# Kernel optimization log

Measured on AMD Instinct MI355X. Metric: run time of the kernel, lower is better.

Reference implementation:

```python
import jax, jax.numpy as jnp
import numpy as np

N_NODES = 32
N_EDGES = N_NODES * (N_NODES - 1)  # 992
BATCH = 16
SEQ = 8
BS = BATCH * SEQ  # 128 frames
D = 256  # node_latent_dim == edge_latent_dim
ITERS = 3


def gru_cell(x, h, Wih, Whh, bih, bhh):
    # torch GRUCell: gates ordered (r, z, n)
    gi = x @ Wih.T + bih
    gh = h @ Whh.T + bhh
    ir, iz, inn = jnp.split(gi, 3, axis=-1)
    hr, hz, hn = jnp.split(gh, 3, axis=-1)
    r = jax.nn.sigmoid(ir + hr)
    z = jax.nn.sigmoid(iz + hz)
    n = jnp.tanh(inn + r * hn)
    return (1.0 - z) * n + z * h


def setup_inputs() -> dict:
    key = jax.random.key(0)
    ks = jax.random.split(key, 16)
    s = 0.05
    inp = {
        'node_latents': jax.random.normal(ks[0], (BS * N_NODES, D), jnp.float32),
        'edge_latents': jax.random.normal(ks[1], (BS * N_EDGES, D), jnp.float32),
        'node_Wih': jax.random.normal(ks[2], (3 * D, D), jnp.float32) * s,
        'node_Whh': jax.random.normal(ks[3], (3 * D, D), jnp.float32) * s,
        'node_bih': jax.random.normal(ks[4], (3 * D,), jnp.float32) * s,
        'node_bhh': jax.random.normal(ks[5], (3 * D,), jnp.float32) * s,
        'edge_Wih': jax.random.normal(ks[6], (3 * D, D), jnp.float32) * s,
        'edge_Whh': jax.random.normal(ks[7], (3 * D, D), jnp.float32) * s,
        'edge_bih': jax.random.normal(ks[8], (3 * D,), jnp.float32) * s,
        'edge_bhh': jax.random.normal(ks[9], (3 * D,), jnp.float32) * s,
        'w_node_pool': jax.random.normal(ks[10], (2 * D,), jnp.float32) * s,
        'w_edge_pool_sub': jax.random.normal(ks[11], (2 * D,), jnp.float32) * s,
        'w_edge_pool_obj': jax.random.normal(ks[12], (2 * D,), jnp.float32) * s,
    }
    # all ordered (subject, object) pairs with subject != object, same for every frame
    pairs = np.array([(i, j) for i in range(N_NODES) for j in range(N_NODES) if i != j], dtype=np.int32)  # [E,2]
    e2n = np.concatenate([np.arange(N_EDGES, dtype=np.int32)[:, None], pairs], axis=1)  # [E,3]
    inp['edge_idx_to_node_idxs'] = jnp.asarray(np.broadcast_to(e2n, (BS, N_EDGES, 3)).copy())
    return inp


def reference(node_latents, edge_latents, node_Wih, node_Whh, node_bih, node_bhh,
              edge_Wih, edge_Whh, edge_bih, edge_bhh,
              w_node_pool, w_edge_pool_sub, w_edge_pool_obj, edge_idx_to_node_idxs):
    sub = edge_idx_to_node_idxs[..., 1].astype(jnp.int32)  # [BS,E]
    obj = edge_idx_to_node_idxs[..., 2].astype(jnp.int32)
    bidx = jnp.arange(BS, dtype=jnp.int32)[:, None]
    sub_flat = (bidx * N_NODES + sub).reshape(-1)  # [BS*E]
    obj_flat = (bidx * N_NODES + obj).reshape(-1)

    # initial GRU call with zero hidden state (torch GRUCell default)
    node_hidden = gru_cell(node_latents, jnp.zeros_like(node_latents), node_Wih, node_Whh, node_bih, node_bhh)
    edge_hidden = gru_cell(edge_latents, jnp.zeros_like(edge_latents), edge_Wih, edge_Whh, edge_bih, edge_bhh)

    for _ in range(ITERS):
        nh = node_hidden.reshape(BS, N_NODES, D)
        eh = edge_hidden.reshape(BS, N_EDGES, D)
        ns = jnp.take_along_axis(nh, sub[:, :, None], axis=1)  # [BS,E,D] subject node feats
        no = jnp.take_along_axis(nh, obj[:, :, None], axis=1)  # [BS,E,D]
        cat_s = jnp.concatenate([ns, eh], axis=-1)  # [BS,E,2D]
        cat_o = jnp.concatenate([no, eh], axis=-1)
        g_node = jax.nn.sigmoid(cat_s @ w_node_pool)[..., None]        # [BS,E,1]
        g_sub = jax.nn.sigmoid(cat_s @ w_edge_pool_sub)[..., None]
        g_obj = jax.nn.sigmoid(cat_o @ w_edge_pool_obj)[..., None]
        # node message: gated edge features scattered to subject and object nodes
        # (equivalent to the dense 0/1 incidence matmul since subject != object per edge)
        msg_e = (g_node * eh).reshape(-1, D)  # [BS*E,D]
        node_msg = (jax.ops.segment_sum(msg_e, sub_flat, num_segments=BS * N_NODES)
                    + jax.ops.segment_sum(msg_e, obj_flat, num_segments=BS * N_NODES))  # [BS*N,D]
        edge_msg = (g_sub * ns + g_obj * no).reshape(-1, D)  # [BS*E,D]
        node_hidden = gru_cell(node_msg, node_hidden, node_Wih, node_Whh, node_bih, node_bhh)
        edge_hidden = gru_cell(edge_msg, edge_hidden, edge_Wih, edge_Whh, edge_bih, edge_bhh)

    return (node_hidden.reshape(BS, N_NODES, D), edge_hidden.reshape(BS, N_EDGES, D))
```

## Files before the change

### kernel.cpp

```cpp
#include <hip/hip_runtime.h>


#define D_DIM 256
#define NNODE 32
#define NEDGE 992
#define EDGE_ROWS (128 * NEDGE)
#define NODE_ROWS (128 * NNODE)
#define BM 64
#define XH_OFF 0
#define HH_OFF 512
#define GI_OFF 32768
#define GI_STR 776

typedef _Float16 half8 __attribute__((ext_vector_type(8)));
typedef __attribute__((ext_vector_type(4))) float f32x4;

__device__ __forceinline__ float sigf(float x) { return 1.0f / (1.0f + __expf(-x)); }
__device__ __forceinline__ float tanh_fast(float x) { return 2.0f / (1.0f + __expf(-2.0f * x)) - 1.0f; }
__device__ __forceinline__ float dot4(float4 a, float4 b) { return a.x*b.x + a.y*b.y + a.z*b.z + a.w*b.w; }

__global__ __launch_bounds__(64) void pack_w(const float* __restrict__ Wih,
                                             const float* __restrict__ Whh,
                                             _Float16* __restrict__ ph) {
  const int ct = blockIdx.x;
  const int ks = blockIdx.y;
  const int l = threadIdx.x;
  const int col = ct * 16 + (l & 15);
  const int kb = ks * 32 + (l >> 4) * 8;
  const float* src = (kb < 256) ? (Wih + col * 256 + kb) : (Whh + col * 256 + (kb - 256));
  half8 v;
  #pragma unroll
  for (int j = 0; j < 8; ++j) v[j] = (_Float16)src[j];
  *(half8*)(ph + ((ct * 16 + ks) * 64 + l) * 8) = v;
}

template <int MODE>
__global__ __launch_bounds__(1024, 4) void gru_mfma(
    const float* __restrict__ xsrc, float* __restrict__ h,
    const _Float16* __restrict__ wp,
    const float* __restrict__ bih, const float* __restrict__ bhh,
    const float* __restrict__ wesb, const float* __restrict__ weob,
    const float* __restrict__ dotS, const float* __restrict__ dotO,
    _Float16* __restrict__ nw) {
  constexpr int RSTR = (MODE == 1) ? 1024 : 512;
  constexpr int LDSB = (MODE == 1) ? 65536 : (MODE == 2 ? 32768 + BM * GI_STR * 2 : 32768);
  __shared__ __align__(16) unsigned char lds[LDSB];

  const int t = threadIdx.x;
  const int rb = blockIdx.x * BM;
  const int srow = t >> 4;
  const int skc = t & 15;
  const int w = t >> 6;
  const int l = t & 63;
  const int lq = l >> 4;
  const int lr = l & 15;
  const int swm = (lr & 7) << 4;
  const int swz = (srow & 7) << 4;
  const int rowg = rb + srow;

  if constexpr (MODE == 2) {
    const int b = rowg / NEDGE;
    const int e = rowg - b * NEDGE;
    const int si = e / 31;
    const int m = e - si * 31;
    const int ob = (m < si) ? m : (m + 1);

    float4 pre[4];
    #pragma unroll
    for (int i = 0; i < 4; ++i)
      pre[i] = *(const float4*)(h + rowg * D_DIM + (i >> 1) * 128 + skc * 8 + (i & 1) * 4);
    #pragma unroll
    for (int c = 0; c < 2; ++c) {
      half8 hh8;
      const float* f1 = (const float*)&pre[c * 2];
      #pragma unroll
      for (int j = 0; j < 8; ++j) hh8[j] = (_Float16)f1[j];
      *(half8*)(&lds[(srow * 512 + c * 256 + skc * 16) ^ swz]) = hh8;
    }
    float pS = 0.f, pO = 0.f;
    #pragma unroll
    for (int i = 0; i < 4; ++i) {
      const int k0 = (i >> 1) * 128 + skc * 8 + (i & 1) * 4;
      pS += dot4(pre[i], *(const float4*)(wesb + k0));
      pO += dot4(pre[i], *(const float4*)(weob + k0));
    }
    #pragma unroll
    for (int mm = 1; mm < 16; mm <<= 1) {
      pS += __shfl_xor(pS, mm, 16);
      pO += __shfl_xor(pO, mm, 16);
    }
    const float gs = sigf(dotS[b * NNODE + si] + pS);
    const float go = sigf(dotO[b * NNODE + ob] + pO);
    const _Float16 gsh = (_Float16)gs, goh = (_Float16)go;
    const _Float16* ns = nw + (b * NNODE + si) * 768;
    const _Float16* no_ = nw + (b * NNODE + ob) * 768;
    _Float16* giw = (_Float16*)(lds + GI_OFF) + srow * GI_STR;
    #pragma unroll
    for (int j = 0; j < 6; ++j) {
      const int c0 = skc * 8 + j * 128;
      const half8 a = *(const half8*)(ns + c0);
      const half8 bb = *(const half8*)(no_ + c0);
      half8 g;
      #pragma unroll
      for (int k = 0; k < 8; ++k) g[k] = gsh * a[k] + goh * bb[k];
      *(half8*)(giw + c0) = g;
    }
  } else if constexpr (MODE != 1) {
    #pragma unroll
    for (int c = 0; c < 2; ++c) {
      half8 hx;
      #pragma unroll
      for (int pq = 0; pq < 2; ++pq) {
        const float4 a = *(const float4*)(xsrc + rowg * D_DIM + c * 128 + skc * 8 + pq * 4);
        hx[pq * 4 + 0] = (_Float16)a.x; hx[pq * 4 + 1] = (_Float16)a.y;
        hx[pq * 4 + 2] = (_Float16)a.z; hx[pq * 4 + 3] = (_Float16)a.w;
      }
      *(half8*)(&lds[(srow * 512 + c * 256 + skc * 16) ^ swz]) = hx;
    }
  } else {
    float4 pre[4];
    #pragma unroll
    for (int i = 0; i < 4; ++i)
      pre[i] = *(const float4*)(h + rowg * D_DIM + (i >> 1) * 128 + skc * 8 + (i & 1) * 4);
    #pragma unroll
    for (int c = 0; c < 2; ++c) {
      half8 hh8;
      const float* f1 = (const float*)&pre[c * 2];
      #pragma unroll
      for (int j = 0; j < 8; ++j) hh8[j] = (_Float16)f1[j];
      *(half8*)(&lds[(srow * RSTR + HH_OFF + c * 256 + skc * 16) ^ swz]) = hh8;
    }
  }

  const f32x4 zz = {0.f, 0.f, 0.f, 0.f};
  f32x4 acc_r[4] = {zz, zz, zz, zz};
  f32x4 acc_z[4] = {zz, zz, zz, zz};
  f32x4 acc_nx[4] = {zz, zz, zz, zz};
  f32x4 acc_nh[4] = {zz, zz, zz, zz};

  auto KS = [&](int hoff, int ksgl, int ksg, f32x4 (&accn)[4]) {
    half8 ah[4];
    #pragma unroll
    for (int rf = 0; rf < 4; ++rf)
      ah[rf] = *(const half8*)(&lds[((rf * 16 + lr) * RSTR + hoff + ksgl * 64 + lq * 16) ^ swm]);
    const half8 br_ = *(const half8*)(wp + (((0 * 16 + w) * 16 + ksg) * 64 + l) * 8);
    const half8 bz_ = *(const half8*)(wp + (((1 * 16 + w) * 16 + ksg) * 64 + l) * 8);
    const half8 bn_ = *(const half8*)(wp + (((2 * 16 + w) * 16 + ksg) * 64 + l) * 8);
    #pragma unroll
    for (int rf = 0; rf < 4; ++rf)
      acc_r[rf] = __builtin_amdgcn_mfma_f32_16x16x32_f16(ah[rf], br_, acc_r[rf], 0, 0, 0);
    #pragma unroll
    for (int rf = 0; rf < 4; ++rf)
      acc_z[rf] = __builtin_amdgcn_mfma_f32_16x16x32_f16(ah[rf], bz_, acc_z[rf], 0, 0, 0);
    #pragma unroll
    for (int rf = 0; rf < 4; ++rf)
      accn[rf] = __builtin_amdgcn_mfma_f32_16x16x32_f16(ah[rf], bn_, accn[rf], 0, 0, 0);
  };

  __syncthreads();

  if constexpr (MODE == 0 || MODE == 3) {
    #pragma unroll
    for (int ksgl = 0; ksgl < 8; ++ksgl) KS(0, ksgl, ksgl, acc_nx);
  } else if constexpr (MODE == 2) {
    #pragma unroll
    for (int ksgl = 0; ksgl < 8; ++ksgl) KS(0, ksgl, 8 + ksgl, acc_nh);
  } else {
    #pragma unroll
    for (int ksgl = 0; ksgl < 8; ++ksgl) KS(HH_OFF, ksgl, 8 + ksgl, acc_nh);
    #pragma unroll
    for (int c = 0; c < 2; ++c) {
      half8 hx;
      #pragma unroll
      for (int pq = 0; pq < 2; ++pq) {
        const float4 a = *(const float4*)(xsrc + rowg * D_DIM + c * 128 + skc * 8 + pq * 4);
        hx[pq * 4 + 0] = (_Float16)a.x; hx[pq * 4 + 1] = (_Float16)a.y;
        hx[pq * 4 + 2] = (_Float16)a.z; hx[pq * 4 + 3] = (_Float16)a.w;
      }
      *(half8*)(&lds[(srow * RSTR + XH_OFF + c * 256 + skc * 16) ^ swz]) = hx;
    }
    __syncthreads();
    #pragma unroll
    for (int ksgl = 0; ksgl < 8; ++ksgl) KS(XH_OFF, ksgl, ksgl, acc_nx);
  }

  const int col = w * 16 + lr;
  if constexpr (MODE == 3) {
    #pragma unroll
    for (int rf = 0; rf < 4; ++rf) {
      #pragma unroll
      for (int q = 0; q < 4; ++q) {
        const int rowl = rf * 16 + lq * 4 + q;
        _Float16* np = nw + (rb + rowl) * 768 + col;
        np[0]   = (_Float16)acc_r[rf][q];
        np[256] = (_Float16)acc_z[rf][q];
        np[512] = (_Float16)acc_nx[rf][q];
      }
    }
    return;
  }
  const float br = bih[col] + bhh[col];
  const float bz = bih[256 + col] + bhh[256 + col];
  const float bnx = bih[512 + col];
  const float bnh = bhh[512 + col];
  if constexpr (MODE == 2) {
    const _Float16* gir = (const _Float16*)(lds + GI_OFF);
    #pragma unroll
    for (int rf = 0; rf < 4; ++rf) {
      #pragma unroll
      for (int q = 0; q < 4; ++q) {
        const int rowl = rf * 16 + lq * 4 + q;
        const _Float16* gp = gir + rowl * GI_STR + col;
        const float r = sigf(acc_r[rf][q] + (float)gp[0] + br);
        const float z = sigf(acc_z[rf][q] + (float)gp[256] + bz);
        const float n = tanh_fast((float)gp[512] + bnx + r * (acc_nh[rf][q] + bnh));
        const float hv = h[(rb + rowl) * D_DIM + col];
        h[(rb + rowl) * D_DIM + col] = (1.0f - z) * n + z * hv;
      }
    }
  } else {
    #pragma unroll
    for (int rf = 0; rf < 4; ++rf) {
      #pragma unroll
      for (int q = 0; q < 4; ++q) {
        const int rowl = rf * 16 + lq * 4 + q;
        const float r = sigf(acc_r[rf][q] + br);
        const float z = sigf(acc_z[rf][q] + bz);
        const float n = tanh_fast(acc_nx[rf][q] + bnx + r * (acc_nh[rf][q] + bnh));
        float hv = 0.0f;
        if constexpr (MODE == 1) hv = h[(rb + rowl) * D_DIM + col];
        h[(rb + rowl) * D_DIM + col] = (1.0f - z) * n + z * hv;
      }
    }
  }
}

__global__ __launch_bounds__(256) void dot3_kernel(
    const float* __restrict__ nh, const float* __restrict__ wnp,
    const float* __restrict__ wes, const float* __restrict__ weo,
    float* __restrict__ dA, float* __restrict__ dS, float* __restrict__ dO) {
  const int r = blockIdx.x * 4 + (threadIdx.x >> 6);
  const int l = threadIdx.x & 63;
  const float4 v = ((const float4*)(nh + r * D_DIM))[l];
  float p1 = dot4(v, ((const float4*)wnp)[l]);
  float p2 = dot4(v, ((const float4*)wes)[l]);
  float p3 = dot4(v, ((const float4*)weo)[l]);
  #pragma unroll
  for (int mm = 32; mm > 0; mm >>= 1) {
    p1 += __shfl_xor(p1, mm, 64);
    p2 += __shfl_xor(p2, mm, 64);
    p3 += __shfl_xor(p3, mm, 64);
  }
  if (l == 0) { dA[r] = p1; dS[r] = p2; dO[r] = p3; }
}

__global__ __launch_bounds__(256) void node_msg_kernel(
    const float* __restrict__ eh, const float* __restrict__ wnp,
    const float* __restrict__ dotA, float* __restrict__ nmsg) {
  __shared__ float sh[3][256];
  const int nr = blockIdx.x;
  const int b = nr >> 5;
  const int n = nr & 31;
  const int wv = threadIdx.x >> 6;
  const int l = threadIdx.x & 63;
  const int base = b * NEDGE;
  const float4 w1b = ((const float4*)(wnp + 256))[l];

  float4 acc = {0.f, 0.f, 0.f, 0.f};
  for (int k = wv; k < 62; k += 4) {
    int e, sub;
    if (k < 31) {
      e = base + n * 31 + k;
      sub = n;
    } else {
      int i = k - 31;
      const int ip = (i < n) ? i : (i + 1);
      e = base + ip * 31 + ((n < ip) ? n : (n - 1));
      sub = ip;
    }
    const float4 ev = ((const float4*)(eh + e * D_DIM))[l];
    float p = dot4(ev, w1b);
    #pragma unroll
    for (int mm = 32; mm > 0; mm >>= 1) p += __shfl_xor(p, mm, 64);
    const float gN = sigf(dotA[b * NNODE + sub] + p);
    acc.x += gN * ev.x; acc.y += gN * ev.y; acc.z += gN * ev.z; acc.w += gN * ev.w;
  }
  if (wv > 0) *(float4*)(&sh[wv - 1][l * 4]) = acc;
  __syncthreads();
  if (wv == 0) {
    #pragma unroll
    for (int v = 0; v < 3; ++v) {
      const float4 o = *(const float4*)(&sh[v][l * 4]);
      acc.x += o.x; acc.y += o.y; acc.z += o.z; acc.w += o.w;
    }
    *(float4*)(nmsg + nr * D_DIM + l * 4) = acc;
  }
}

extern "C" void kernel_launch(void* const* d_in, const int* in_sizes, int n_in,
                              void* d_out, int out_size, void* d_ws, size_t ws_size,
                              hipStream_t stream) {
  const float* node_latents = (const float*)d_in[0];
  const float* edge_latents = (const float*)d_in[1];
  const float* node_Wih = (const float*)d_in[2];
  const float* node_Whh = (const float*)d_in[3];
  const float* node_bih = (const float*)d_in[4];
  const float* node_bhh = (const float*)d_in[5];
  const float* edge_Wih = (const float*)d_in[6];
  const float* edge_Whh = (const float*)d_in[7];
  const float* edge_bih = (const float*)d_in[8];
  const float* edge_bhh = (const float*)d_in[9];
  const float* w_node_pool = (const float*)d_in[10];
  const float* w_edge_sub = (const float*)d_in[11];
  const float* w_edge_obj = (const float*)d_in[12];

  float* nh = (float*)d_out;
  float* eh = (float*)d_out + NODE_ROWS * D_DIM;

  const int WPLANE = 48 * 16 * 64 * 8;
  _Float16* ph_n = (_Float16*)d_ws;
  _Float16* ph_e = ph_n + WPLANE;
  _Float16* NW = ph_e + WPLANE;
  float* fw = (float*)(NW + NODE_ROWS * 768);
  float* dotA = fw; fw += NODE_ROWS;
  float* dotS = fw; fw += NODE_ROWS;
  float* dotO = fw; fw += NODE_ROWS;
  float* node_msg = fw; fw += NODE_ROWS * D_DIM;

  dim3 pg(48, 16);
  pack_w<<<pg, 64, 0, stream>>>(node_Wih, node_Whh, ph_n);
  pack_w<<<pg, 64, 0, stream>>>(edge_Wih, edge_Whh, ph_e);

  gru_mfma<0><<<NODE_ROWS / BM, 1024, 0, stream>>>(
      node_latents, nh, ph_n, node_bih, node_bhh,
      nullptr, nullptr, nullptr, nullptr, nullptr);
  gru_mfma<0><<<EDGE_ROWS / BM, 1024, 0, stream>>>(
      edge_latents, eh, ph_e, edge_bih, edge_bhh,
      nullptr, nullptr, nullptr, nullptr, nullptr);

  for (int it = 0; it < 3; ++it) {
    dot3_kernel<<<NODE_ROWS / 4, 256, 0, stream>>>(nh, w_node_pool, w_edge_sub,
                                                   w_edge_obj, dotA, dotS, dotO);
    gru_mfma<3><<<NODE_ROWS / BM, 1024, 0, stream>>>(
        nh, nullptr, ph_e, nullptr, nullptr,
        nullptr, nullptr, nullptr, nullptr, NW);
    node_msg_kernel<<<NODE_ROWS, 256, 0, stream>>>(eh, w_node_pool, dotA, node_msg);
    gru_mfma<2><<<EDGE_ROWS / BM, 1024, 0, stream>>>(
        nullptr, eh, ph_e, edge_bih, edge_bhh,
        w_edge_sub + 256, w_edge_obj + 256, dotS, dotO, NW);
    gru_mfma<1><<<NODE_ROWS / BM, 1024, 0, stream>>>(
        node_msg, nh, ph_n, node_bih, node_bhh,
        nullptr, nullptr, nullptr, nullptr, nullptr);
  }
}
```

Before: 744.0 us.

## Merge node/edge GRU launches into combined grids and fuse pooling dots

The edge and node initial GRU launches become one grid, and the per-iteration edge and node GRU updates become one grid with a block-index branch. The pooling dot products move into the node-weight projection kernel, so the separate dot3 kernel goes away. This removes several launches per iteration and lets the small node work run alongside the large edge work. In exchange, the combined kernel reserves the larger edge LDS footprint for node blocks too, which may lower occupancy, and the branches add code size.

Result: faster. 715.6 us (-3.8%).

```diff
diff --git a/kernel.cpp b/kernel.cpp
--- a/kernel.cpp
+++ b/kernel.cpp
@@ -7,8 +7,8 @@
 #define EDGE_ROWS (128 * NEDGE)
 #define NODE_ROWS (128 * NNODE)
 #define BM 64
-#define XH_OFF 0
-#define HH_OFF 512
+#define EGRID (EDGE_ROWS / BM)
+#define NGRID (NODE_ROWS / BM)
 #define GI_OFF 32768
 #define GI_STR 776
 
@@ -34,18 +34,96 @@
   *(half8*)(ph + ((ct * 16 + ks) * 64 + l) * 8) = v;
 }
 
-template <int MODE>
-__global__ __launch_bounds__(1024, 4) void gru_mfma(
-    const float* __restrict__ xsrc, float* __restrict__ h,
-    const _Float16* __restrict__ wp,
-    const float* __restrict__ bih, const float* __restrict__ bhh,
-    const float* __restrict__ wesb, const float* __restrict__ weob,
-    const float* __restrict__ dotS, const float* __restrict__ dotO,
-    _Float16* __restrict__ nw) {
-  constexpr int RSTR = (MODE == 1) ? 1024 : 512;
-  constexpr int LDSB = (MODE == 1) ? 65536 : (MODE == 2 ? 32768 + BM * GI_STR * 2 : 32768);
-  __shared__ __align__(16) unsigned char lds[LDSB];
-
+__global__ __launch_bounds__(1024, 4) void gru_init(
+    const float* __restrict__ xe, const float* __restrict__ xn,
+    float* __restrict__ he, float* __restrict__ hn,
+    const _Float16* __restrict__ wpe, const _Float16* __restrict__ wpn,
+    const float* __restrict__ ebih, const float* __restrict__ ebhh,
+    const float* __restrict__ nbih, const float* __restrict__ nbhh) {
+  __shared__ __align__(16) unsigned char lds[32768];
+  const bool edge = blockIdx.x < EGRID;
+  const int bx = edge ? blockIdx.x : (blockIdx.x - EGRID);
+  const float* xsrc = edge ? xe : xn;
+  float* h = edge ? he : hn;
+  const _Float16* wp = edge ? wpe : wpn;
+  const float* bih = edge ? ebih : nbih;
+  const float* bhh = edge ? ebhh : nbhh;
+
+  const int t = threadIdx.x;
+  const int rb = bx * BM;
+  const int srow = t >> 4;
+  const int skc = t & 15;
+  const int w = t >> 6;
+  const int l = t & 63;
+  const int lq = l >> 4;
+  const int lr = l & 15;
+  const int swm = (lr & 7) << 4;
+  const int swz = (srow & 7) << 4;
+  const int rowg = rb + srow;
+
+  #pragma unroll
+  for (int c = 0; c < 2; ++c) {
+    half8 hx;
+    #pragma unroll
+    for (int pq = 0; pq < 2; ++pq) {
+      const float4 a = *(const float4*)(xsrc + rowg * D_DIM + c * 128 + skc * 8 + pq * 4);
+      hx[pq * 4 + 0] = (_Float16)a.x; hx[pq * 4 + 1] = (_Float16)a.y;
+      hx[pq * 4 + 2] = (_Float16)a.z; hx[pq * 4 + 3] = (_Float16)a.w;
+    }
+    *(half8*)(&lds[(srow * 512 + c * 256 + skc * 16) ^ swz]) = hx;
+  }
+  __syncthreads();
+
+  const f32x4 zz = {0.f, 0.f, 0.f, 0.f};
+  f32x4 acc_r[4] = {zz, zz, zz, zz};
+  f32x4 acc_z[4] = {zz, zz, zz, zz};
+  f32x4 acc_nx[4] = {zz, zz, zz, zz};
+
+  #pragma unroll
+  for (int ksg = 0; ksg < 8; ++ksg) {
+    half8 ah[4];
+    #pragma unroll
+    for (int rf = 0; rf < 4; ++rf)
+      ah[rf] = *(const half8*)(&lds[((rf * 16 + lr) * 512 + ksg * 64 + lq * 16) ^ swm]);
+    const half8 br_ = *(const half8*)(wp + (((0 * 16 + w) * 16 + ksg) * 64 + l) * 8);
+    const half8 bz_ = *(const half8*)(wp + (((1 * 16 + w) * 16 + ksg) * 64 + l) * 8);
+    const half8 bn_ = *(const half8*)(wp + (((2 * 16 + w) * 16 + ksg) * 64 + l) * 8);
+    #pragma unroll
+    for (int rf = 0; rf < 4; ++rf)
+      acc_r[rf] = __builtin_amdgcn_mfma_f32_16x16x32_f16(ah[rf], br_, acc_r[rf], 0, 0, 0);
+    #pragma unroll
+    for (int rf = 0; rf < 4; ++rf)
+      acc_z[rf] = __builtin_amdgcn_mfma_f32_16x16x32_f16(ah[rf], bz_, acc_z[rf], 0, 0, 0);
+    #pragma unroll
+    for (int rf = 0; rf < 4; ++rf)
+      acc_nx[rf] = __builtin_amdgcn_mfma_f32_16x16x32_f16(ah[rf], bn_, acc_nx[rf], 0, 0, 0);
+  }
+
+  const int col = w * 16 + lr;
+  const float br = bih[col] + bhh[col];
+  const float bz = bih[256 + col] + bhh[256 + col];
+  const float bnx = bih[512 + col];
+  const float bnh = bhh[512 + col];
+  #pragma unroll
+  for (int rf = 0; rf < 4; ++rf) {
+    #pragma unroll
+    for (int q = 0; q < 4; ++q) {
+      const int rowl = rf * 16 + lq * 4 + q;
+      const float r = sigf(acc_r[rf][q] + br);
+      const float z = sigf(acc_z[rf][q] + bz);
+      const float n = tanh_fast(acc_nx[rf][q] + bnx + r * bnh);
+      h[(rb + rowl) * D_DIM + col] = (1.0f - z) * n;
+    }
+  }
+}
+
+__global__ __launch_bounds__(1024, 4) void gru_nw(
+    const float* __restrict__ nh, const _Float16* __restrict__ wp,
+    _Float16* __restrict__ nw,
+    const float* __restrict__ wnp, const float* __restrict__ wes,
+    const float* __restrict__ weo,
+    float* __restrict__ dA, float* __restrict__ dS, float* __restrict__ dO) {
+  __shared__ __align__(16) unsigned char lds[32768];
   const int t = threadIdx.x;
   const int rb = blockIdx.x * BM;
   const int srow = t >> 4;
@@ -58,7 +136,104 @@
   const int swz = (srow & 7) << 4;
   const int rowg = rb + srow;
 
-  if constexpr (MODE == 2) {
+  float4 xa[4];
+  #pragma unroll
+  for (int i = 0; i < 4; ++i)
+    xa[i] = *(const float4*)(nh + rowg * D_DIM + (i >> 1) * 128 + skc * 8 + (i & 1) * 4);
+  #pragma unroll
+  for (int c = 0; c < 2; ++c) {
+    half8 hx;
+    const float* f0 = (const float*)&xa[c * 2];
+    #pragma unroll
+    for (int j = 0; j < 8; ++j) hx[j] = (_Float16)f0[j];
+    *(half8*)(&lds[(srow * 512 + c * 256 + skc * 16) ^ swz]) = hx;
+  }
+  float p1 = 0.f, p2 = 0.f, p3 = 0.f;
+  #pragma unroll
+  for (int i = 0; i < 4; ++i) {
+    const int k0 = (i >> 1) * 128 + skc * 8 + (i & 1) * 4;
+    p1 += dot4(xa[i], *(const float4*)(wnp + k0));
+    p2 += dot4(xa[i], *(const float4*)(wes + k0));
+    p3 += dot4(xa[i], *(const float4*)(weo + k0));
+  }
+  #pragma unroll
+  for (int mm = 1; mm < 16; mm <<= 1) {
+    p1 += __shfl_xor(p1, mm, 16);
+    p2 += __shfl_xor(p2, mm, 16);
+    p3 += __shfl_xor(p3, mm, 16);
+  }
+  if (skc == 0) { dA[rowg] = p1; dS[rowg] = p2; dO[rowg] = p3; }
+  __syncthreads();
+
+  const f32x4 zz = {0.f, 0.f, 0.f, 0.f};
+  f32x4 acc_r[4] = {zz, zz, zz, zz};
+  f32x4 acc_z[4] = {zz, zz, zz, zz};
+  f32x4 acc_nx[4] = {zz, zz, zz, zz};
+
+  #pragma unroll
+  for (int ksg = 0; ksg < 8; ++ksg) {
+    half8 ah[4];
+    #pragma unroll
+    for (int rf = 0; rf < 4; ++rf)
+      ah[rf] = *(const half8*)(&lds[((rf * 16 + lr) * 512 + ksg * 64 + lq * 16) ^ swm]);
+    const half8 br_ = *(const half8*)(wp + (((0 * 16 + w) * 16 + ksg) * 64 + l) * 8);
+    const half8 bz_ = *(const half8*)(wp + (((1 * 16 + w) * 16 + ksg) * 64 + l) * 8);
+    const half8 bn_ = *(const half8*)(wp + (((2 * 16 + w) * 16 + ksg) * 64 + l) * 8);
+    #pragma unroll
+    for (int rf = 0; rf < 4; ++rf)
+      acc_r[rf] = __builtin_amdgcn_mfma_f32_16x16x32_f16(ah[rf], br_, acc_r[rf], 0, 0, 0);
+    #pragma unroll
+    for (int rf = 0; rf < 4; ++rf)
+      acc_z[rf] = __builtin_amdgcn_mfma_f32_16x16x32_f16(ah[rf], bz_, acc_z[rf], 0, 0, 0);
+    #pragma unroll
+    for (int rf = 0; rf < 4; ++rf)
+      acc_nx[rf] = __builtin_amdgcn_mfma_f32_16x16x32_f16(ah[rf], bn_, acc_nx[rf], 0, 0, 0);
+  }
+
+  const int col = w * 16 + lr;
+  #pragma unroll
+  for (int rf = 0; rf < 4; ++rf) {
+    #pragma unroll
+    for (int q = 0; q < 4; ++q) {
+      const int rowl = rf * 16 + lq * 4 + q;
+      _Float16* np = nw + (rb + rowl) * 768 + col;
+      np[0]   = (_Float16)acc_r[rf][q];
+      np[256] = (_Float16)acc_z[rf][q];
+      np[512] = (_Float16)acc_nx[rf][q];
+    }
+  }
+}
+
+__global__ __launch_bounds__(1024, 4) void gru_iter(
+    float* __restrict__ eh, float* __restrict__ nh,
+    const float* __restrict__ nmsg,
+    const _Float16* __restrict__ wpe, const _Float16* __restrict__ wpn,
+    const float* __restrict__ ebih, const float* __restrict__ ebhh,
+    const float* __restrict__ nbih, const float* __restrict__ nbhh,
+    const float* __restrict__ wesb, const float* __restrict__ weob,
+    const float* __restrict__ dotS, const float* __restrict__ dotO,
+    const _Float16* __restrict__ nw) {
+  __shared__ __align__(16) unsigned char lds[32768 + BM * GI_STR * 2];
+
+  const int t = threadIdx.x;
+  const int srow = t >> 4;
+  const int skc = t & 15;
+  const int w = t >> 6;
+  const int l = t & 63;
+  const int lq = l >> 4;
+  const int lr = l & 15;
+  const int swm = (lr & 7) << 4;
+  const int swz = (srow & 7) << 4;
+
+  const f32x4 zz = {0.f, 0.f, 0.f, 0.f};
+  f32x4 acc_r[4] = {zz, zz, zz, zz};
+  f32x4 acc_z[4] = {zz, zz, zz, zz};
+  f32x4 acc_nx[4] = {zz, zz, zz, zz};
+  f32x4 acc_nh[4] = {zz, zz, zz, zz};
+
+  if (blockIdx.x < EGRID) {
+    const int rb = blockIdx.x * BM;
+    const int rowg = rb + srow;
     const int b = rowg / NEDGE;
     const int e = rowg - b * NEDGE;
     const int si = e / 31;
@@ -68,7 +243,7 @@
     float4 pre[4];
     #pragma unroll
     for (int i = 0; i < 4; ++i)
-      pre[i] = *(const float4*)(h + rowg * D_DIM + (i >> 1) * 128 + skc * 8 + (i & 1) * 4);
+      pre[i] = *(const float4*)(eh + rowg * D_DIM + (i >> 1) * 128 + skc * 8 + (i & 1) * 4);
     #pragma unroll
     for (int c = 0; c < 2; ++c) {
       half8 hh8;
@@ -105,105 +280,34 @@
       for (int k = 0; k < 8; ++k) g[k] = gsh * a[k] + goh * bb[k];
       *(half8*)(giw + c0) = g;
     }
-  } else if constexpr (MODE != 1) {
-    #pragma unroll
-    for (int c = 0; c < 2; ++c) {
-      half8 hx;
-      #pragma unroll
-      for (int pq = 0; pq < 2; ++pq) {
-        const float4 a = *(const float4*)(xsrc + rowg * D_DIM + c * 128 + skc * 8 + pq * 4);
-        hx[pq * 4 + 0] = (_Float16)a.x; hx[pq * 4 + 1] = (_Float16)a.y;
-        hx[pq * 4 + 2] = (_Float16)a.z; hx[pq * 4 + 3] = (_Float16)a.w;
-      }
-      *(half8*)(&lds[(srow * 512 + c * 256 + skc * 16) ^ swz]) = hx;
-    }
-  } else {
-    float4 pre[4];
-    #pragma unroll
-    for (int i = 0; i < 4; ++i)
-      pre[i] = *(const float4*)(h + rowg * D_DIM + (i >> 1) * 128 + skc * 8 + (i & 1) * 4);
-    #pragma unroll
-    for (int c = 0; c < 2; ++c) {
-      half8 hh8;
-      const float* f1 = (const float*)&pre[c * 2];
-      #pragma unroll
-      for (int j = 0; j < 8; ++j) hh8[j] = (_Float16)f1[j];
-      *(half8*)(&lds[(srow * RSTR + HH_OFF + c * 256 + skc * 16) ^ swz]) = hh8;
-    }
-  }
-
-  const f32x4 zz = {0.f, 0.f, 0.f, 0.f};
-  f32x4 acc_r[4] = {zz, zz, zz, zz};
-  f32x4 acc_z[4] = {zz, zz, zz, zz};
-  f32x4 acc_nx[4] = {zz, zz, zz, zz};
-  f32x4 acc_nh[4] = {zz, zz, zz, zz};
-
-  auto KS = [&](int hoff, int ksgl, int ksg, f32x4 (&accn)[4]) {
-    half8 ah[4];
-    #pragma unroll
-    for (int rf = 0; rf < 4; ++rf)
-      ah[rf] = *(const half8*)(&lds[((rf * 16 + lr) * RSTR + hoff + ksgl * 64 + lq * 16) ^ swm]);
-    const half8 br_ = *(const half8*)(wp + (((0 * 16 + w) * 16 + ksg) * 64 + l) * 8);
-    const half8 bz_ = *(const half8*)(wp + (((1 * 16 + w) * 16 + ksg) * 64 + l) * 8);
-    const half8 bn_ = *(const half8*)(wp + (((2 * 16 + w) * 16 + ksg) * 64 + l) * 8);
-    #pragma unroll
-    for (int rf = 0; rf < 4; ++rf)
-      acc_r[rf] = __builtin_amdgcn_mfma_f32_16x16x32_f16(ah[rf], br_, acc_r[rf], 0, 0, 0);
-    #pragma unroll
-    for (int rf = 0; rf < 4; ++rf)
-      acc_z[rf] = __builtin_amdgcn_mfma_f32_16x16x32_f16(ah[rf], bz_, acc_z[rf], 0, 0, 0);
-    #pragma unroll
-    for (int rf = 0; rf < 4; ++rf)
-      accn[rf] = __builtin_amdgcn_mfma_f32_16x16x32_f16(ah[rf], bn_, accn[rf], 0, 0, 0);
-  };
-
-  __syncthreads();
-
-  if constexpr (MODE == 0 || MODE == 3) {
-    #pragma unroll
-    for (int ksgl = 0; ksgl < 8; ++ksgl) KS(0, ksgl, ksgl, acc_nx);
-  } else if constexpr (MODE == 2) {
-    #pragma unroll
-    for (int ksgl = 0; ksgl < 8; ++ksgl) KS(0, ksgl, 8 + ksgl, acc_nh);
-  } else {
-    #pragma unroll
-    for (int ksgl = 0; ksgl < 8; ++ksgl) KS(HH_OFF, ksgl, 8 + ksgl, acc_nh);
-    #pragma unroll
-    for (int c = 0; c < 2; ++c) {
-      half8 hx;
-      #pragma unroll
-      for (int pq = 0; pq < 2; ++pq) {
-        const float4 a = *(const float4*)(xsrc + rowg * D_DIM + c * 128 + skc * 8 + pq * 4);
-        hx[pq * 4 + 0] = (_Float16)a.x; hx[pq * 4 + 1] = (_Float16)a.y;
-        hx[pq * 4 + 2] = (_Float16)a.z; hx[pq * 4 + 3] = (_Float16)a.w;
-      }
-      *(half8*)(&lds[(srow * RSTR + XH_OFF + c * 256 + skc * 16) ^ swz]) = hx;
-    }
     __syncthreads();
-    #pragma unroll
-    for (int ksgl = 0; ksgl < 8; ++ksgl) KS(XH_OFF, ksgl, ksgl, acc_nx);
-  }
-
-  const int col = w * 16 + lr;
-  if constexpr (MODE == 3) {
-    #pragma unroll
-    for (int rf = 0; rf < 4; ++rf) {
-      #pragma unroll
-      for (int q = 0; q < 4; ++q) {
-        const int rowl = rf * 16 + lq * 4 + q;
-        _Float16* np = nw + (rb + rowl) * 768 + col;
-        np[0]   = (_Float16)acc_r[rf][q];
-        np[256] = (_Float16)acc_z[rf][q];
-        np[512] = (_Float16)acc_nx[rf][q];
-      }
-    }
-    return;
-  }
-  const float br = bih[col] + bhh[col];
-  const float bz = bih[256 + col] + bhh[256 + col];
-  const float bnx = bih[512 + col];
-  const float bnh = bhh[512 + col];
-  if constexpr (MODE == 2) {
+
+    #pragma unroll
+    for (int ksg = 0; ksg < 8; ++ksg) {
+      half8 ah[4];
+      #pragma unroll
+      for (int rf = 0; rf < 4; ++rf)
+        ah[rf] = *(const half8*)(&lds[((rf * 16 + lr) * 512 + ksg * 64 + lq * 16) ^ swm]);
+      const int kk = 8 + ksg;
+      const half8 br_ = *(const half8*)(wpe + (((0 * 16 + w) * 16 + kk) * 64 + l) * 8);
+      const half8 bz_ = *(const half8*)(wpe + (((1 * 16 + w) * 16 + kk) * 64 + l) * 8);
+      const half8 bn_ = *(const half8*)(wpe + (((2 * 16 + w) * 16 + kk) * 64 + l) * 8);
+      #pragma unroll
+      for (int rf = 0; rf < 4; ++rf)
+        acc_r[rf] = __builtin_amdgcn_mfma_f32_16x16x32_f16(ah[rf], br_, acc_r[rf], 0, 0, 0);
+      #pragma unroll
+      for (int rf = 0; rf < 4; ++rf)
+        acc_z[rf] = __builtin_amdgcn_mfma_f32_16x16x32_f16(ah[rf], bz_, acc_z[rf], 0, 0, 0);
+      #pragma unroll
+      for (int rf = 0; rf < 4; ++rf)
+        acc_nh[rf] = __builtin_amdgcn_mfma_f32_16x16x32_f16(ah[rf], bn_, acc_nh[rf], 0, 0, 0);
+    }
+
+    const int col = w * 16 + lr;
+    const float br = ebih[col] + ebhh[col];
+    const float bz = ebih[256 + col] + ebhh[256 + col];
+    const float bnx = ebih[512 + col];
+    const float bnh = ebhh[512 + col];
     const _Float16* gir = (const _Float16*)(lds + GI_OFF);
     #pragma unroll
     for (int rf = 0; rf < 4; ++rf) {
@@ -214,11 +318,88 @@
         const float r = sigf(acc_r[rf][q] + (float)gp[0] + br);
         const float z = sigf(acc_z[rf][q] + (float)gp[256] + bz);
         const float n = tanh_fast((float)gp[512] + bnx + r * (acc_nh[rf][q] + bnh));
-        const float hv = h[(rb + rowl) * D_DIM + col];
-        h[(rb + rowl) * D_DIM + col] = (1.0f - z) * n + z * hv;
+        const float hv = eh[(rb + rowl) * D_DIM + col];
+        eh[(rb + rowl) * D_DIM + col] = (1.0f - z) * n + z * hv;
       }
     }
   } else {
+    const int rb = (blockIdx.x - EGRID) * BM;
+    const int rowg = rb + srow;
+
+    {
+      float4 pre[4];
+      #pragma unroll
+      for (int i = 0; i < 4; ++i)
+        pre[i] = *(const float4*)(nh + rowg * D_DIM + (i >> 1) * 128 + skc * 8 + (i & 1) * 4);
+      #pragma unroll
+      for (int c = 0; c < 2; ++c) {
+        half8 hh8;
+        const float* f1 = (const float*)&pre[c * 2];
+        #pragma unroll
+        for (int j = 0; j < 8; ++j) hh8[j] = (_Float16)f1[j];
+        *(half8*)(&lds[(srow * 1024 + 512 + c * 256 + skc * 16) ^ swz]) = hh8;
+      }
+    }
+    __syncthreads();
+
+    #pragma unroll
+    for (int ksg = 0; ksg < 8; ++ksg) {
+      half8 ah[4];
+      #pragma unroll
+      for (int rf = 0; rf < 4; ++rf)
+        ah[rf] = *(const half8*)(&lds[((rf * 16 + lr) * 1024 + 512 + ksg * 64 + lq * 16) ^ swm]);
+      const int kk = 8 + ksg;
+      const half8 br_ = *(const half8*)(wpn + (((0 * 16 + w) * 16 + kk) * 64 + l) * 8);
+      const half8 bz_ = *(const half8*)(wpn + (((1 * 16 + w) * 16 + kk) * 64 + l) * 8);
+      const half8 bn_ = *(const half8*)(wpn + (((2 * 16 + w) * 16 + kk) * 64 + l) * 8);
+      #pragma unroll
+      for (int rf = 0; rf < 4; ++rf)
+        acc_r[rf] = __builtin_amdgcn_mfma_f32_16x16x32_f16(ah[rf], br_, acc_r[rf], 0, 0, 0);
+      #pragma unroll
+      for (int rf = 0; rf < 4; ++rf)
+        acc_z[rf] = __builtin_amdgcn_mfma_f32_16x16x32_f16(ah[rf], bz_, acc_z[rf], 0, 0, 0);
+      #pragma unroll
+      for (int rf = 0; rf < 4; ++rf)
+        acc_nh[rf] = __builtin_amdgcn_mfma_f32_16x16x32_f16(ah[rf], bn_, acc_nh[rf], 0, 0, 0);
+    }
+
+    #pragma unroll
+    for (int c = 0; c < 2; ++c) {
+      half8 hx;
+      #pragma unroll
+      for (int pq = 0; pq < 2; ++pq) {
+        const float4 a = *(const float4*)(nmsg + rowg * D_DIM + c * 128 + skc * 8 + pq * 4);
+        hx[pq * 4 + 0] = (_Float16)a.x; hx[pq * 4 + 1] = (_Float16)a.y;
+        hx[pq * 4 + 2] = (_Float16)a.z; hx[pq * 4 + 3] = (_Float16)a.w;
+      }
+      *(half8*)(&lds[(srow * 1024 + 0 + c * 256 + skc * 16) ^ swz]) = hx;
+    }
+    __syncthreads();
+    #pragma unroll
+    for (int ksg = 0; ksg < 8; ++ksg) {
+      half8 ah[4];
+      #pragma unroll
+      for (int rf = 0; rf < 4; ++rf)
+        ah[rf] = *(const half8*)(&lds[((rf * 16 + lr) * 1024 + 0 + ksg * 64 + lq * 16) ^ swm]);
+      const half8 br_ = *(const half8*)(wpn + (((0 * 16 + w) * 16 + ksg) * 64 + l) * 8);
+      const half8 bz_ = *(const half8*)(wpn + (((1 * 16 + w) * 16 + ksg) * 64 + l) * 8);
+      const half8 bn_ = *(const half8*)(wpn + (((2 * 16 + w) * 16 + ksg) * 64 + l) * 8);
+      #pragma unroll
+      for (int rf = 0; rf < 4; ++rf)
+        acc_r[rf] = __builtin_amdgcn_mfma_f32_16x16x32_f16(ah[rf], br_, acc_r[rf], 0, 0, 0);
+      #pragma unroll
+      for (int rf = 0; rf < 4; ++rf)
+        acc_z[rf] = __builtin_amdgcn_mfma_f32_16x16x32_f16(ah[rf], bz_, acc_z[rf], 0, 0, 0);
+      #pragma unroll
+      for (int rf = 0; rf < 4; ++rf)
+        acc_nx[rf] = __builtin_amdgcn_mfma_f32_16x16x32_f16(ah[rf], bn_, acc_nx[rf], 0, 0, 0);
+    }
+
+    const int col = w * 16 + lr;
+    const float br = nbih[col] + nbhh[col];
+    const float bz = nbih[256 + col] + nbhh[256 + col];
+    const float bnx = nbih[512 + col];
+    const float bnh = nbhh[512 + col];
     #pragma unroll
     for (int rf = 0; rf < 4; ++rf) {
       #pragma unroll
@@ -227,31 +408,11 @@
         const float r = sigf(acc_r[rf][q] + br);
         const float z = sigf(acc_z[rf][q] + bz);
         const float n = tanh_fast(acc_nx[rf][q] + bnx + r * (acc_nh[rf][q] + bnh));
-        float hv = 0.0f;
-        if constexpr (MODE == 1) hv = h[(rb + rowl) * D_DIM + col];
-        h[(rb + rowl) * D_DIM + col] = (1.0f - z) * n + z * hv;
+        const float hv = nh[(rb + rowl) * D_DIM + col];
+        nh[(rb + rowl) * D_DIM + col] = (1.0f - z) * n + z * hv;
       }
     }
   }
-}
-
-__global__ __launch_bounds__(256) void dot3_kernel(
-    const float* __restrict__ nh, const float* __restrict__ wnp,
-    const float* __restrict__ wes, const float* __restrict__ weo,
-    float* __restrict__ dA, float* __restrict__ dS, float* __restrict__ dO) {
-  const int r = blockIdx.x * 4 + (threadIdx.x >> 6);
-  const int l = threadIdx.x & 63;
-  const float4 v = ((const float4*)(nh + r * D_DIM))[l];
-  float p1 = dot4(v, ((const float4*)wnp)[l]);
-  float p2 = dot4(v, ((const float4*)wes)[l]);
-  float p3 = dot4(v, ((const float4*)weo)[l]);
-  #pragma unroll
-  for (int mm = 32; mm > 0; mm >>= 1) {
-    p1 += __shfl_xor(p1, mm, 64);
-    p2 += __shfl_xor(p2, mm, 64);
-    p3 += __shfl_xor(p3, mm, 64);
-  }
-  if (l == 0) { dA[r] = p1; dS[r] = p2; dO[r] = p3; }
 }
 
 __global__ __launch_bounds__(256) void node_msg_kernel(
@@ -331,25 +492,17 @@
   pack_w<<<pg, 64, 0, stream>>>(node_Wih, node_Whh, ph_n);
   pack_w<<<pg, 64, 0, stream>>>(edge_Wih, edge_Whh, ph_e);
 
-  gru_mfma<0><<<NODE_ROWS / BM, 1024, 0, stream>>>(
-      node_latents, nh, ph_n, node_bih, node_bhh,
-      nullptr, nullptr, nullptr, nullptr, nullptr);
-  gru_mfma<0><<<EDGE_ROWS / BM, 1024, 0, stream>>>(
-      edge_latents, eh, ph_e, edge_bih, edge_bhh,
-      nullptr, nullptr, nullptr, nullptr, nullptr);
+  gru_init<<<EGRID + NGRID, 1024, 0, stream>>>(
+      edge_latents, node_latents, eh, nh, ph_e, ph_n,
+      edge_bih, edge_bhh, node_bih, node_bhh);
 
   for (int it = 0; it < 3; ++it) {
-    dot3_kernel<<<NODE_ROWS / 4, 256, 0, stream>>>(nh, w_node_pool, w_edge_sub,
-                                                   w_edge_obj, dotA, dotS, dotO);
-    gru_mfma<3><<<NODE_ROWS / BM, 1024, 0, stream>>>(
-        nh, nullptr, ph_e, nullptr, nullptr,
-        nullptr, nullptr, nullptr, nullptr, NW);
+    gru_nw<<<NGRID, 1024, 0, stream>>>(
+        nh, ph_e, NW, w_node_pool, w_edge_sub, w_edge_obj, dotA, dotS, dotO);
     node_msg_kernel<<<NODE_ROWS, 256, 0, stream>>>(eh, w_node_pool, dotA, node_msg);
-    gru_mfma<2><<<EDGE_ROWS / BM, 1024, 0, stream>>>(
-        nullptr, eh, ph_e, edge_bih, edge_bhh,
+    gru_iter<<<EGRID + NGRID, 1024, 0, stream>>>(
+        eh, nh, node_msg, ph_e, ph_n,
+        edge_bih, edge_bhh, node_bih, node_bhh,
         w_edge_sub + 256, w_edge_obj + 256, dotS, dotO, NW);
-    gru_mfma<1><<<NODE_ROWS / BM, 1024, 0, stream>>>(
-        node_msg, nh, ph_n, node_bih, node_bhh,
-        nullptr, nullptr, nullptr, nullptr, nullptr);
   }
 }
```
